# Kernel optimization log

Measured on AMD Instinct MI355X. Metric: run time of the kernel, lower is better.

The kernel has to match this reference:

```python
import jax, jax.numpy as jnp
import numpy as np
from jax import lax

NUM_HEADS = 4
ROPE_BASE = 10000.0


def _rope(x):
    # x: (b, h, w, c). Faithful to the torch RoPE: angles indexed by the h axis
    # with shape (h, c/2), which broadcasts against the w axis (requires h == w).
    b, h, w, c = x.shape
    k_max = c // 2
    theta = 1.0 / (ROPE_BASE ** (jnp.arange(k_max, dtype=x.dtype) / k_max))  # (c/2,)
    angles = jnp.arange(h, dtype=x.dtype)[:, None] * theta  # (h, c/2)
    cos, sin = jnp.cos(angles), jnp.sin(angles)
    xr = x.reshape(b, h, w, k_max, 2)
    re, im = xr[..., 0], xr[..., 1]
    # complex multiply (cos + i sin) * (re + i im); (h, c/2) broadcasts along w
    out_re = cos * re - sin * im
    out_im = sin * re + cos * im
    return jnp.stack([out_re, out_im], axis=-1).reshape(b, h, w, c)


def setup_inputs() -> dict:
    key = jax.random.key(0)
    k1, k2, k3, k4, k5 = jax.random.split(key, 5)
    b, c, h, w = 8, 512, 96, 96
    x = jax.random.normal(k1, (b, c, h, w), dtype=jnp.float32)
    W_qk = jax.random.normal(k2, (2 * c, c), dtype=jnp.float32) * (c ** -0.5)
    b_qk = jax.random.normal(k3, (2 * c,), dtype=jnp.float32) * 0.02
    lepe_w = jax.random.normal(k4, (c, 1, 3, 3), dtype=jnp.float32) * (1.0 / 3.0)
    lepe_b = jax.random.normal(k5, (c,), dtype=jnp.float32) * 0.02
    return {"x": x, "W_qk": W_qk, "b_qk": b_qk, "lepe_w": lepe_w, "lepe_b": lepe_b}


def reference(x, W_qk, b_qk, lepe_w, lepe_b):
    b, c, h, w = x.shape
    n = h * w
    heads = NUM_HEADS
    hd = c // heads

    xs = x.reshape(b, c, n).transpose(0, 2, 1)  # (b, n, c)
    qk = (xs @ W_qk.T + b_qk).reshape(b, n, 2, c)
    q = jax.nn.elu(qk[:, :, 0]) + 1.0  # (b, n, c)
    k = jax.nn.elu(qk[:, :, 1]) + 1.0
    v = xs

    q_rope = _rope(q.reshape(b, h, w, c)).reshape(b, n, heads, hd).transpose(0, 2, 1, 3)
    k_rope = _rope(k.reshape(b, h, w, c)).reshape(b, n, heads, hd).transpose(0, 2, 1, 3)

    # faithful flat reshape (b, n, c) -> (b, heads, n, hd) (splits the n axis)
    q2 = q.reshape(b, heads, n, hd)
    k2 = k.reshape(b, heads, n, hd)
    v2 = v.reshape(b, heads, n, hd)

    k_mean = k2.mean(axis=2, keepdims=True)  # (b, heads, 1, hd)
    z = 1.0 / (jnp.einsum('bhnd,bhmd->bhnm', q2, k_mean) + 1e-6)  # (b, heads, n, 1)

    scale = n ** -0.5
    kv = jnp.einsum('bhnd,bhne->bhde', k_rope * scale, v2 * scale)  # (b, heads, hd, hd)
    out = jnp.einsum('bhnd,bhde->bhne', q_rope, kv) * z  # (b, heads, n, hd)

    out = out.transpose(0, 2, 1, 3).reshape(b, n, c).transpose(0, 2, 1).reshape(b, c, h, w)

    # v2.reshape(b,h,w,c).permute(0,3,1,2) recovers the original (b, c, h, w) layout
    v_img = v2.reshape(b, h, w, c).transpose(0, 3, 1, 2)
    lepe = lax.conv_general_dilated(
        v_img, lepe_w, window_strides=(1, 1), padding='SAME',
        feature_group_count=c, dimension_numbers=('NCHW', 'OIHW', 'NCHW'))
    lepe = lepe + lepe_b[None, :, None, None]
    return out + lepe
```

## Files before the change

### kernel.cpp

```cpp
#include <hip/hip_runtime.h>
#include <hip/hip_bf16.h>
#include <cstdint>

#define BB 8
#define CC 512
#define HH 96
#define NN 9216
#define HEADS 4
#define HD 128
#define KMAX 256

typedef unsigned short ushort_t;
typedef __attribute__((ext_vector_type(8))) short bf16x8;
typedef __attribute__((ext_vector_type(4))) float f32x4;

__device__ __forceinline__ unsigned short f2bf(float f) {
  unsigned int u = __float_as_uint(f);
  u += 0x7fffu + ((u >> 16) & 1u);
  return (unsigned short)(u >> 16);
}
__device__ __forceinline__ float bf2f(unsigned short s) {
  return __uint_as_float(((unsigned int)s) << 16);
}
__device__ __forceinline__ unsigned int pk2(float lo, float hi) {
  return (unsigned int)f2bf(lo) | ((unsigned int)f2bf(hi) << 16);
}

__device__ __forceinline__ void gld16(const void* g, void* l) {
  __builtin_amdgcn_global_load_lds(
      (const __attribute__((address_space(1))) unsigned int*)(uintptr_t)g,
      (__attribute__((address_space(3))) unsigned int*)(unsigned int)(uintptr_t)l,
      16, 0, 0);
}

__global__ void rope_table_k(float* __restrict__ rope) {
  int t = blockIdx.x * 256 + threadIdx.x;
  if (t >= HH * KMAX) return;
  int col = t >> 8;
  int kk = t & (KMAX - 1);
  float theta = powf(10000.0f, -((float)kk) / (float)KMAX);
  float ang = (float)col * theta;
  float s, c;
  sincosf(ang, &s, &c);
  rope[2 * t] = c;
  rope[2 * t + 1] = s;
}

__global__ void conv_w_k(const float* __restrict__ W, unsigned short* __restrict__ Wbf) {
  int t = blockIdx.x * 256 + threadIdx.x;
  float4 v = *(const float4*)(W + (size_t)t * 4);
  unsigned int lo = (unsigned int)f2bf(v.x) | ((unsigned int)f2bf(v.y) << 16);
  unsigned int hi = (unsigned int)f2bf(v.z) | ((unsigned int)f2bf(v.w) << 16);
  *(uint2*)(Wbf + (size_t)t * 4) = make_uint2(lo, hi);
}

__global__ void transpose_all_k(const float* __restrict__ x, unsigned short* __restrict__ xt) {
  __shared__ unsigned short T[64 * 72];
  const int pos0 = blockIdx.x * 64;
  const int ch0 = blockIdx.y * 64;
  const int b = blockIdx.z;
  const int tid = threadIdx.x;
#pragma unroll
  for (int i = 0; i < 4; ++i) {
    int fi = i * 256 + tid;
    int ch = fi >> 4, p4 = fi & 15;
    float4 v = *(const float4*)(x + ((size_t)b * CC + ch0 + ch) * NN + pos0 + p4 * 4);
    T[(p4 * 4 + 0) * 72 + ch] = f2bf(v.x);
    T[(p4 * 4 + 1) * 72 + ch] = f2bf(v.y);
    T[(p4 * 4 + 2) * 72 + ch] = f2bf(v.z);
    T[(p4 * 4 + 3) * 72 + ch] = f2bf(v.w);
  }
  __syncthreads();
#pragma unroll
  for (int i = 0; i < 2; ++i) {
    int s = i * 256 + tid;
    int p = s >> 3, cc = s & 7;
    uint4 u = *(const uint4*)&T[p * 72 + cc * 8];
    *(uint4*)(xt + ((size_t)b * NN + pos0 + p) * CC + ch0 + cc * 8) = u;
  }
}

__launch_bounds__(256)
__global__ void gemm_qk_mfma(const unsigned short* __restrict__ xtall,
                             const unsigned short* __restrict__ Wbf,
                             const float* __restrict__ bqk,
                             unsigned short* __restrict__ qout,
                             unsigned short* __restrict__ kout) {
  __shared__ __align__(16) unsigned short sA[128 * 64];
  __shared__ __align__(16) unsigned short sB[128 * 64];
  const int flat = blockIdx.x;
  const int bn = (flat >> 3) & 7;
  const int g = ((flat >> 6) << 3) | (flat & 7);
  const int b = g / 72;
  const int m0 = (g - b * 72) * 128;
  const int tid = threadIdx.x;
  const int wv = tid >> 6, lane = tid & 63;
  const int j0 = bn * 128;
  const unsigned short* xt = xtall + (size_t)b * NN * CC;
  const int row = lane & 15, quad = lane >> 4;
  const int mt0 = (wv & 1) * 64, nt0 = (wv >> 1) * 64;
  f32x4 acc[4][4];
#pragma unroll
  for (int mi = 0; mi < 4; ++mi)
#pragma unroll
    for (int ni = 0; ni < 4; ++ni) acc[mi][ni] = (f32x4){0.f, 0.f, 0.f, 0.f};

  for (int kt = 0; kt < CC; kt += 64) {
#pragma unroll
    for (int it = 0; it < 4; ++it) {
      int s = it * 256 + tid;
      int srow = s >> 3;
      int sc = (s & 7) ^ (srow & 7);
      int ldsoff = (it * 256 + wv * 64) * 8;
      gld16(xt + (size_t)(m0 + srow) * CC + kt + sc * 8, &sA[ldsoff]);
      gld16(Wbf + (size_t)(j0 + srow) * CC + kt + sc * 8, &sB[ldsoff]);
    }
    __syncthreads();
#pragma unroll
    for (int ks = 0; ks < 2; ++ks) {
      bf16x8 af[4], bf[4];
      const int chunk = (ks * 4 + quad) ^ (row & 7);
#pragma unroll
      for (int mi = 0; mi < 4; ++mi)
        af[mi] = *(const bf16x8*)&sA[((mt0 + mi * 16 + row) * 8 + chunk) * 8];
#pragma unroll
      for (int ni = 0; ni < 4; ++ni)
        bf[ni] = *(const bf16x8*)&sB[((nt0 + ni * 16 + row) * 8 + chunk) * 8];
#pragma unroll
      for (int mi = 0; mi < 4; ++mi)
#pragma unroll
        for (int ni = 0; ni < 4; ++ni)
          acc[mi][ni] = __builtin_amdgcn_mfma_f32_16x16x32_bf16(af[mi], bf[ni], acc[mi][ni], 0, 0, 0);
    }
    __syncthreads();
  }
  unsigned short* dst = (j0 < CC) ? qout : kout;
  const int jl = (j0 & (CC - 1)) + nt0;
  float bj[4];
#pragma unroll
  for (int ni = 0; ni < 4; ++ni) bj[ni] = bqk[j0 + nt0 + ni * 16 + row];
#pragma unroll
  for (int mi = 0; mi < 4; ++mi) {
#pragma unroll
    for (int ni = 0; ni < 4; ++ni) {
#pragma unroll
      for (int r = 0; r < 4; ++r) {
        float v = acc[mi][ni][r] + bj[ni];
        v = v > 0.f ? v + 1.f : expm1f(v) + 1.f;
        int mrow = m0 + mt0 + mi * 16 + quad * 4 + r;
        dst[((size_t)b * NN + mrow) * CC + jl + ni * 16 + row] = f2bf(v);
      }
    }
  }
}

__global__ void kmean_p1_k(const unsigned short* __restrict__ kbf, float* __restrict__ part) {
  __shared__ float red[256];
  const int seg = blockIdx.x;
  const int bh = blockIdx.y;
  const int b = bh >> 2, head = bh & 3;
  const int tid = threadIdx.x;
  const int d = tid & 127, half = tid >> 7;
  const unsigned short* base =
      kbf + ((size_t)b * NN + head * 2304 + seg * 128 + half * 64) * CC + d;
  float sum = 0.f;
  for (int pp = 0; pp < 64; ++pp) {
    const unsigned short* rp = base + (size_t)pp * CC;
    sum += bf2f(rp[0]) + bf2f(rp[128]) + bf2f(rp[256]) + bf2f(rp[384]);
  }
  red[tid] = sum;
  __syncthreads();
  if (half == 0) part[((size_t)bh * 18 + seg) * 128 + d] = red[d] + red[d + 128];
}

__global__ void kmean_p2_k(const float* __restrict__ part, float* __restrict__ kmean) {
  int idx = blockIdx.x * 256 + threadIdx.x;
  int bh = idx >> 7, d = idx & 127;
  float s = 0.f;
#pragma unroll
  for (int i = 0; i < 18; ++i) s += part[((size_t)bh * 18 + i) * 128 + d];
  kmean[idx] = s * (1.0f / 9216.0f);
}

__global__ void z_k(const unsigned short* __restrict__ qbf, const float* __restrict__ kmean,
                    float* __restrict__ z) {
  const int wv = threadIdx.x >> 6, lane = threadIdx.x & 63;
  const int zbase = (blockIdx.x * 4 + wv) * 8;
  const int bh = zbase / NN;
  const int p0 = zbase % NN;
  const int b = bh >> 2, head = bh & 3;
  const float km0 = kmean[bh * 128 + lane * 2];
  const float km1 = kmean[bh * 128 + lane * 2 + 1];
#pragma unroll
  for (int it = 0; it < 8; ++it) {
    const int p = p0 + it;
    const int pos = head * 2304 + (p >> 2);
    const int chb = (p & 3) * 128;
    const unsigned short* qp = qbf + ((size_t)b * NN + pos) * CC + chb + lane * 2;
    float dot = bf2f(qp[0]) * km0 + bf2f(qp[1]) * km1;
#pragma unroll
    for (int off = 1; off < 64; off <<= 1) dot += __shfl_xor(dot, off, 64);
    if (lane == 0) z[zbase + it] = 1.0f / (dot + 1e-6f);
  }
}

__launch_bounds__(256, 2)
__global__ void kv_mfma_k(const unsigned short* __restrict__ kbf, const float* __restrict__ x,
                          const float* __restrict__ rope, float* __restrict__ kvp) {
  __shared__ __align__(16) unsigned short sK[128 * 64];
  const int s = blockIdx.x;
  const int bh = blockIdx.y;
  const int b = bh >> 2, head = bh & 3;
  const int tid = threadIdx.x;
  const int wv = tid >> 6, lane = tid & 63;
  const int row = lane & 15, quad = lane >> 4;
  const int e0 = (wv & 1) * 64, d0 = (wv >> 1) * 64;
  const int r = s >> 2;
  const int t0 = (s & 3) * 576;

  const int qg = tid & 7;
  const int dg = (tid >> 3) * 4;
  const unsigned short* kbase = kbf + (size_t)b * NN * CC + head * HD + dg;
  const int pairb = head * 64 + (dg >> 1);

  f32x4 acc[4][4];
#pragma unroll
  for (int mi = 0; mi < 4; ++mi)
#pragma unroll
    for (int ni = 0; ni < 4; ++ni) acc[mi][ni] = (f32x4){0.f, 0.f, 0.f, 0.f};

  for (int ck = 0; ck < 9; ++ck) {
    const int tc = t0 + ck * 64;
    float4 a0[8], a1[8];
#pragma unroll
    for (int mi = 0; mi < 4; ++mi)
#pragma unroll
      for (int ks = 0; ks < 2; ++ks) {
        const float* xp = x + (size_t)(b * CC + r * 128 + e0 + mi * 16 + row) * NN +
                          head * 2304 + tc + ks * 32 + quad * 8;
        a0[mi * 2 + ks] = *(const float4*)xp;
        a1[mi * 2 + ks] = *(const float4*)(xp + 4);
      }
    {
      int p = 4 * (tc + qg * 8) + r;
      int col = p % 96;
      float rw0[8], rw1[8], rw2[8], rw3[8];
#pragma unroll
      for (int j = 0; j < 8; ++j) {
        uint2 kv2 = *(const uint2*)(kbase + (size_t)p * CC);
        const float* rp = rope + ((size_t)col * KMAX + pairb) * 2;
        float4 cs = *(const float4*)rp;
        float re0 = bf2f((unsigned short)(kv2.x & 0xffffu));
        float im0 = bf2f((unsigned short)(kv2.x >> 16));
        float re1 = bf2f((unsigned short)(kv2.y & 0xffffu));
        float im1 = bf2f((unsigned short)(kv2.y >> 16));
        rw0[j] = cs.x * re0 - cs.y * im0;
        rw1[j] = cs.y * re0 + cs.x * im0;
        rw2[j] = cs.z * re1 - cs.w * im1;
        rw3[j] = cs.w * re1 + cs.z * im1;
        p += 4;
        col += 4;
        col = (col >= 96) ? col - 96 : col;
      }
#pragma unroll
      for (int rr = 0; rr < 4; ++rr) {
        const float* rw = (rr == 0) ? rw0 : (rr == 1) ? rw1 : (rr == 2) ? rw2 : rw3;
        const int d = dg + rr;
        uint4 pk;
        pk.x = pk2(rw[0], rw[1]);
        pk.y = pk2(rw[2], rw[3]);
        pk.z = pk2(rw[4], rw[5]);
        pk.w = pk2(rw[6], rw[7]);
        *(uint4*)&sK[(d * 8 + (qg ^ (d & 7))) * 8] = pk;
      }
    }
    __syncthreads();
#pragma unroll
    for (int ks = 0; ks < 2; ++ks) {
      bf16x8 bfr[4];
#pragma unroll
      for (int ni = 0; ni < 4; ++ni) {
        const int d = d0 + ni * 16 + row;
        const int o = (ks * 4 + quad) ^ (d & 7);
        bfr[ni] = *(const bf16x8*)&sK[(d * 8 + o) * 8];
      }
#pragma unroll
      for (int mi = 0; mi < 4; ++mi) {
        const int f = mi * 2 + ks;
        union { bf16x8 v; unsigned int u[4]; } af;
        af.u[0] = pk2(a0[f].x, a0[f].y);
        af.u[1] = pk2(a0[f].z, a0[f].w);
        af.u[2] = pk2(a1[f].x, a1[f].y);
        af.u[3] = pk2(a1[f].z, a1[f].w);
#pragma unroll
        for (int ni = 0; ni < 4; ++ni)
          acc[mi][ni] = __builtin_amdgcn_mfma_f32_16x16x32_bf16(af.v, bfr[ni], acc[mi][ni], 0, 0, 0);
      }
    }
    __syncthreads();
  }
  float* dst = kvp + (size_t)(s * 32 + bh) * (HD * HD);
#pragma unroll
  for (int mi = 0; mi < 4; ++mi) {
#pragma unroll
    for (int ni = 0; ni < 4; ++ni) {
#pragma unroll
      for (int rr = 0; rr < 4; ++rr) {
        const int e = e0 + mi * 16 + quad * 4 + rr;
        const int d = d0 + ni * 16 + row;
        dst[e * HD + d] = acc[mi][ni][rr];
      }
    }
  }
}

__global__ void kv_reduce_k(const float* __restrict__ kvp, unsigned short* __restrict__ kvtb) {
  int idx = blockIdx.x * 256 + threadIdx.x;
  float ssum = 0.f;
#pragma unroll
  for (int i = 0; i < 16; ++i) ssum += kvp[(size_t)i * (32 * HD * HD) + idx];
  kvtb[idx] = f2bf(ssum * (1.0f / 9216.0f));
}

__launch_bounds__(256)
__global__ void out_mfma_k(const unsigned short* __restrict__ qbf,
                           const unsigned short* __restrict__ kvtb,
                           const float* __restrict__ z, const float* __restrict__ rope,
                           float* __restrict__ out) {
  const int bh = blockIdx.y, b = bh >> 2, head = bh & 3;
  const int pos0 = blockIdx.x * 128;
  const int tid = threadIdx.x, wv = tid >> 6, lane = tid & 63;
  const int row = lane & 15, quad = lane >> 4;
  const int e0 = (wv & 1) * 64;
  const int p0 = (wv >> 1) * 64;
  f32x4 acc[4][4];
#pragma unroll
  for (int mi = 0; mi < 4; ++mi)
#pragma unroll
    for (int ni = 0; ni < 4; ++ni) acc[mi][ni] = (f32x4){0.f, 0.f, 0.f, 0.f};

  int posn[4], coln[4];
#pragma unroll
  for (int ni = 0; ni < 4; ++ni) {
    posn[ni] = pos0 + p0 + ni * 16 + row;
    coln[ni] = posn[ni] % 96;
  }

#pragma unroll
  for (int kt = 0; kt < HD; kt += 32) {
    bf16x8 af[4], bfr[4];
#pragma unroll
    for (int mi = 0; mi < 4; ++mi)
      af[mi] = *(const bf16x8*)&kvtb[((size_t)bh * HD + e0 + mi * 16 + row) * HD + kt + quad * 8];
#pragma unroll
    for (int ni = 0; ni < 4; ++ni) {
      const uint4 u = *(const uint4*)(qbf + ((size_t)b * NN + posn[ni]) * CC +
                                      head * HD + kt + quad * 8);
      const int pairb = head * 64 + (kt >> 1) + quad * 4;
      const float* rp = rope + ((size_t)coln[ni] * KMAX + pairb) * 2;
      float4 r0 = *(const float4*)rp;
      float4 r1 = *(const float4*)(rp + 4);
      unsigned int uu[4] = {u.x, u.y, u.z, u.w};
      float cs[8] = {r0.x, r0.y, r0.z, r0.w, r1.x, r1.y, r1.z, r1.w};
      bf16x8 bb;
#pragma unroll
      for (int pr = 0; pr < 4; ++pr) {
        float re = bf2f((unsigned short)(uu[pr] & 0xffffu));
        float im = bf2f((unsigned short)(uu[pr] >> 16));
        float c = cs[2 * pr], s = cs[2 * pr + 1];
        bb[2 * pr] = (short)f2bf(c * re - s * im);
        bb[2 * pr + 1] = (short)f2bf(s * re + c * im);
      }
      bfr[ni] = bb;
    }
#pragma unroll
    for (int mi = 0; mi < 4; ++mi)
#pragma unroll
      for (int ni = 0; ni < 4; ++ni)
        acc[mi][ni] = __builtin_amdgcn_mfma_f32_16x16x32_bf16(af[mi], bfr[ni], acc[mi][ni], 0, 0, 0);
  }
  float zv[4];
#pragma unroll
  for (int ni = 0; ni < 4; ++ni) zv[ni] = z[(size_t)bh * NN + posn[ni]];
#pragma unroll
  for (int mi = 0; mi < 4; ++mi) {
#pragma unroll
    for (int ni = 0; ni < 4; ++ni) {
#pragma unroll
      for (int r = 0; r < 4; ++r) {
        int e = e0 + mi * 16 + quad * 4 + r;
        out[((size_t)b * CC + head * HD + e) * NN + posn[ni]] = acc[mi][ni][r] * zv[ni];
      }
    }
  }
}

__global__ void lepe_k(const float* __restrict__ x, const float* __restrict__ lw,
                       const float* __restrict__ lb, float* __restrict__ out) {
  const int blk = blockIdx.x;
  const int bc = blk / 9;
  const int tile = blk - bc * 9;
  const int ch = bc & (CC - 1);
  const float* wp = lw + ch * 9;
  float w[9];
#pragma unroll
  for (int t = 0; t < 9; ++t) w[t] = wp[t];
  const float bias = lb[ch];
  const float* xp = x + (size_t)bc * NN;
  const int pos = tile * 1024 + threadIdx.x * 4;
  const int pi = pos / 96;
  const int pj = pos - pi * 96;

  float4 o = *(const float4*)(out + (size_t)bc * NN + pos);

  float a0 = bias, a1 = bias, a2 = bias, a3 = bias;
#pragma unroll
  for (int r = 0; r < 3; ++r) {
    const int y = pi + r - 1;
    if ((unsigned)y >= 96u) continue;
    const float* rowp = xp + y * 96 + pj;
    float4 M = *(const float4*)rowp;
    float Lv = (pj > 0) ? rowp[-1] : 0.f;
    float Rv = (pj < 92) ? rowp[4] : 0.f;
    const float w0 = w[r * 3 + 0], w1 = w[r * 3 + 1], w2 = w[r * 3 + 2];
    a0 += w0 * Lv + w1 * M.x + w2 * M.y;
    a1 += w0 * M.x + w1 * M.y + w2 * M.z;
    a2 += w0 * M.y + w1 * M.z + w2 * M.w;
    a3 += w0 * M.z + w1 * M.w + w2 * Rv;
  }
  o.x += a0; o.y += a1; o.z += a2; o.w += a3;
  *(float4*)(out + (size_t)bc * NN + pos) = o;
}

extern "C" void kernel_launch(void* const* d_in, const int* in_sizes, int n_in,
                              void* d_out, int out_size, void* d_ws, size_t ws_size,
                              hipStream_t stream) {
  const float* x = (const float*)d_in[0];
  const float* Wqk = (const float*)d_in[1];
  const float* bqk = (const float*)d_in[2];
  const float* lw = (const float*)d_in[3];
  const float* lb = (const float*)d_in[4];
  float* out = (float*)d_out;
  char* ws = (char*)d_ws;
  unsigned short* qbf = (unsigned short*)(ws);
  unsigned short* kbf = (unsigned short*)(ws + 75497472);
  float* rope = (float*)(ws + 150994944);
  float* kmean = (float*)(ws + 151191552);
  float* z = (float*)(ws + 151207936);
  float* kvp = (float*)(ws + 152387584);
  float* kmean_part = (float*)(ws + 152387584 + 16777216);
  unsigned short* kvtb = (unsigned short*)(ws + 185942016);
  unsigned short* Wbf = (unsigned short*)(ws + 188039168);
  unsigned short* xtb = (unsigned short*)d_out;

  conv_w_k<<<dim3(512), dim3(256), 0, stream>>>(Wqk, Wbf);
  rope_table_k<<<dim3(96), dim3(256), 0, stream>>>(rope);
  transpose_all_k<<<dim3(144, 8, 8), dim3(256), 0, stream>>>(x, xtb);
  gemm_qk_mfma<<<dim3(4608), dim3(256), 0, stream>>>(xtb, Wbf, bqk, qbf, kbf);
  kmean_p1_k<<<dim3(18, 32), dim3(256), 0, stream>>>(kbf, kmean_part);
  kmean_p2_k<<<dim3(16), dim3(256), 0, stream>>>(kmean_part, kmean);
  z_k<<<dim3(9216), dim3(256), 0, stream>>>(qbf, kmean, z);
  kv_mfma_k<<<dim3(16, 32), dim3(256), 0, stream>>>(kbf, x, rope, kvp);
  kv_reduce_k<<<dim3(2048), dim3(256), 0, stream>>>(kvp, kvtb);
  out_mfma_k<<<dim3(72, 32), dim3(256), 0, stream>>>(qbf, kvtb, z, rope, out);
  lepe_k<<<dim3(36864), dim3(256), 0, stream>>>(x, lw, lb, out);
}
```

Baseline: 723.2 us.

## Fuse k-mean reduction into QK GEMM epilogue and stage out_mfma through LDS

The QK GEMM swaps its operand roles so each lane holds four consecutive channels. That allows packed 8-byte bf16 stores and lets the kernel accumulate per-channel sums of k with shuffles and atomics, which replaces the two separate k-mean reduction kernels. The output kernel now loads its q tile into swizzled LDS once, and it transposes the result through LDS so the stores to the channel-major output are coalesced float4 writes instead of scattered scalar stores. This adds a memset, atomic contention, and extra barriers in the output kernel.

Result: no change. 713.2 us (-1.4%).

```diff
diff --git a/kernel.cpp b/kernel.cpp
--- a/kernel.cpp
+++ b/kernel.cpp
@@ -85,7 +85,8 @@
                              const unsigned short* __restrict__ Wbf,
                              const float* __restrict__ bqk,
                              unsigned short* __restrict__ qout,
-                             unsigned short* __restrict__ kout) {
+                             unsigned short* __restrict__ kout,
+                             float* __restrict__ ksum) {
   __shared__ __align__(16) unsigned short sA[128 * 64];
   __shared__ __align__(16) unsigned short sB[128 * 64];
   const int flat = blockIdx.x;
@@ -98,12 +99,12 @@
   const int j0 = bn * 128;
   const unsigned short* xt = xtall + (size_t)b * NN * CC;
   const int row = lane & 15, quad = lane >> 4;
-  const int mt0 = (wv & 1) * 64, nt0 = (wv >> 1) * 64;
+  const int jt0 = (wv & 1) * 64, pt0 = (wv >> 1) * 64;
   f32x4 acc[4][4];
 #pragma unroll
-  for (int mi = 0; mi < 4; ++mi)
-#pragma unroll
-    for (int ni = 0; ni < 4; ++ni) acc[mi][ni] = (f32x4){0.f, 0.f, 0.f, 0.f};
+  for (int ji = 0; ji < 4; ++ji)
+#pragma unroll
+    for (int pi = 0; pi < 4; ++pi) acc[ji][pi] = (f32x4){0.f, 0.f, 0.f, 0.f};
 
   for (int kt = 0; kt < CC; kt += 64) {
 #pragma unroll
@@ -118,79 +119,69 @@
     __syncthreads();
 #pragma unroll
     for (int ks = 0; ks < 2; ++ks) {
-      bf16x8 af[4], bf[4];
+      bf16x8 aw[4], ax[4];
       const int chunk = (ks * 4 + quad) ^ (row & 7);
 #pragma unroll
-      for (int mi = 0; mi < 4; ++mi)
-        af[mi] = *(const bf16x8*)&sA[((mt0 + mi * 16 + row) * 8 + chunk) * 8];
-#pragma unroll
-      for (int ni = 0; ni < 4; ++ni)
-        bf[ni] = *(const bf16x8*)&sB[((nt0 + ni * 16 + row) * 8 + chunk) * 8];
-#pragma unroll
-      for (int mi = 0; mi < 4; ++mi)
-#pragma unroll
-        for (int ni = 0; ni < 4; ++ni)
-          acc[mi][ni] = __builtin_amdgcn_mfma_f32_16x16x32_bf16(af[mi], bf[ni], acc[mi][ni], 0, 0, 0);
+      for (int ji = 0; ji < 4; ++ji)
+        aw[ji] = *(const bf16x8*)&sB[((jt0 + ji * 16 + row) * 8 + chunk) * 8];
+#pragma unroll
+      for (int pi = 0; pi < 4; ++pi)
+        ax[pi] = *(const bf16x8*)&sA[((pt0 + pi * 16 + row) * 8 + chunk) * 8];
+#pragma unroll
+      for (int ji = 0; ji < 4; ++ji)
+#pragma unroll
+        for (int pi = 0; pi < 4; ++pi)
+          acc[ji][pi] = __builtin_amdgcn_mfma_f32_16x16x32_bf16(aw[ji], ax[pi], acc[ji][pi], 0, 0, 0);
     }
     __syncthreads();
   }
   unsigned short* dst = (j0 < CC) ? qout : kout;
-  const int jl = (j0 & (CC - 1)) + nt0;
-  float bj[4];
-#pragma unroll
-  for (int ni = 0; ni < 4; ++ni) bj[ni] = bqk[j0 + nt0 + ni * 16 + row];
-#pragma unroll
-  for (int mi = 0; mi < 4; ++mi) {
-#pragma unroll
-    for (int ni = 0; ni < 4; ++ni) {
+  const int jl0 = j0 & (CC - 1);
+  const int pq = (m0 >> 7) / 18;
+#pragma unroll
+  for (int ji = 0; ji < 4; ++ji) {
+    const float4 bb = *(const float4*)&bqk[j0 + jt0 + ji * 16 + quad * 4];
+    const float bj[4] = {bb.x, bb.y, bb.z, bb.w};
+    float sacc[4] = {0.f, 0.f, 0.f, 0.f};
+#pragma unroll
+    for (int pi = 0; pi < 4; ++pi) {
+      float v[4];
 #pragma unroll
       for (int r = 0; r < 4; ++r) {
-        float v = acc[mi][ni][r] + bj[ni];
-        v = v > 0.f ? v + 1.f : expm1f(v) + 1.f;
-        int mrow = m0 + mt0 + mi * 16 + quad * 4 + r;
-        dst[((size_t)b * NN + mrow) * CC + jl + ni * 16 + row] = f2bf(v);
-      }
-    }
-  }
-}
-
-__global__ void kmean_p1_k(const unsigned short* __restrict__ kbf, float* __restrict__ part) {
-  __shared__ float red[256];
-  const int seg = blockIdx.x;
-  const int bh = blockIdx.y;
-  const int b = bh >> 2, head = bh & 3;
-  const int tid = threadIdx.x;
-  const int d = tid & 127, half = tid >> 7;
-  const unsigned short* base =
-      kbf + ((size_t)b * NN + head * 2304 + seg * 128 + half * 64) * CC + d;
-  float sum = 0.f;
-  for (int pp = 0; pp < 64; ++pp) {
-    const unsigned short* rp = base + (size_t)pp * CC;
-    sum += bf2f(rp[0]) + bf2f(rp[128]) + bf2f(rp[256]) + bf2f(rp[384]);
-  }
-  red[tid] = sum;
-  __syncthreads();
-  if (half == 0) part[((size_t)bh * 18 + seg) * 128 + d] = red[d] + red[d + 128];
-}
-
-__global__ void kmean_p2_k(const float* __restrict__ part, float* __restrict__ kmean) {
-  int idx = blockIdx.x * 256 + threadIdx.x;
-  int bh = idx >> 7, d = idx & 127;
-  float s = 0.f;
-#pragma unroll
-  for (int i = 0; i < 18; ++i) s += part[((size_t)bh * 18 + i) * 128 + d];
-  kmean[idx] = s * (1.0f / 9216.0f);
-}
-
-__global__ void z_k(const unsigned short* __restrict__ qbf, const float* __restrict__ kmean,
+        float t = acc[ji][pi][r] + bj[r];
+        v[r] = t > 0.f ? t + 1.f : __expf(t);
+        sacc[r] += v[r];
+      }
+      const int posm = m0 + pt0 + pi * 16 + row;
+      uint2 pkd = make_uint2(pk2(v[0], v[1]), pk2(v[2], v[3]));
+      *(uint2*)&dst[((size_t)b * NN + posm) * CC + jl0 + jt0 + ji * 16 + quad * 4] = pkd;
+    }
+    if (j0 >= CC) {
+#pragma unroll
+      for (int r = 0; r < 4; ++r) {
+        float s = sacc[r];
+        s += __shfl_xor(s, 1);
+        s += __shfl_xor(s, 2);
+        s += __shfl_xor(s, 4);
+        s += __shfl_xor(s, 8);
+        if (row == 0)
+          atomicAdd(&ksum[((size_t)b * 4 + pq) * 512 + jl0 + jt0 + ji * 16 + quad * 4 + r], s);
+      }
+    }
+  }
+}
+
+__global__ void z_k(const unsigned short* __restrict__ qbf, const float* __restrict__ ksum,
                     float* __restrict__ z) {
   const int wv = threadIdx.x >> 6, lane = threadIdx.x & 63;
   const int zbase = (blockIdx.x * 4 + wv) * 8;
   const int bh = zbase / NN;
   const int p0 = zbase % NN;
   const int b = bh >> 2, head = bh & 3;
-  const float km0 = kmean[bh * 128 + lane * 2];
-  const float km1 = kmean[bh * 128 + lane * 2 + 1];
+  const float* ks = ksum + (size_t)bh * 512;
+  const int d0 = lane * 2;
+  const float km0 = (ks[d0] + ks[d0 + 128] + ks[d0 + 256] + ks[d0 + 384]) * (1.0f / 9216.0f);
+  const float km1 = (ks[d0 + 1] + ks[d0 + 129] + ks[d0 + 257] + ks[d0 + 385]) * (1.0f / 9216.0f);
 #pragma unroll
   for (int it = 0; it < 8; ++it) {
     const int p = p0 + it;
@@ -327,12 +318,24 @@
                            const unsigned short* __restrict__ kvtb,
                            const float* __restrict__ z, const float* __restrict__ rope,
                            float* __restrict__ out) {
+  __shared__ __align__(16) float Ts[64 * 132];
+  unsigned short* sQ = (unsigned short*)Ts;
   const int bh = blockIdx.y, b = bh >> 2, head = bh & 3;
   const int pos0 = blockIdx.x * 128;
   const int tid = threadIdx.x, wv = tid >> 6, lane = tid & 63;
   const int row = lane & 15, quad = lane >> 4;
   const int e0 = (wv & 1) * 64;
   const int p0 = (wv >> 1) * 64;
+
+#pragma unroll
+  for (int it = 0; it < 8; ++it) {
+    const int s = it * 256 + tid;
+    const int srow = s >> 4, sc = s & 15;
+    const int scs = (sc & 8) | ((sc & 7) ^ (srow & 7));
+    gld16(qbf + ((size_t)b * NN + pos0 + srow) * CC + head * HD + scs * 8,
+          &sQ[(size_t)(it * 256 + wv * 64) * 8]);
+  }
+
   f32x4 acc[4][4];
 #pragma unroll
   for (int mi = 0; mi < 4; ++mi)
@@ -345,6 +348,7 @@
     posn[ni] = pos0 + p0 + ni * 16 + row;
     coln[ni] = posn[ni] % 96;
   }
+  __syncthreads();
 
 #pragma unroll
   for (int kt = 0; kt < HD; kt += 32) {
@@ -354,8 +358,10 @@
       af[mi] = *(const bf16x8*)&kvtb[((size_t)bh * HD + e0 + mi * 16 + row) * HD + kt + quad * 8];
 #pragma unroll
     for (int ni = 0; ni < 4; ++ni) {
-      const uint4 u = *(const uint4*)(qbf + ((size_t)b * NN + posn[ni]) * CC +
-                                      head * HD + kt + quad * 8);
+      const int posL = p0 + ni * 16 + row;
+      const int chb = (kt >> 3) + quad;
+      const int cl = (chb & 8) | ((chb & 7) ^ (posL & 7));
+      const uint4 u = *(const uint4*)&sQ[posL * 128 + cl * 8];
       const int pairb = head * 64 + (kt >> 1) + quad * 4;
       const float* rp = rope + ((size_t)coln[ni] * KMAX + pairb) * 2;
       float4 r0 = *(const float4*)rp;
@@ -379,19 +385,39 @@
       for (int ni = 0; ni < 4; ++ni)
         acc[mi][ni] = __builtin_amdgcn_mfma_f32_16x16x32_bf16(af[mi], bfr[ni], acc[mi][ni], 0, 0, 0);
   }
-  float zv[4];
-#pragma unroll
-  for (int ni = 0; ni < 4; ++ni) zv[ni] = z[(size_t)bh * NN + posn[ni]];
-#pragma unroll
-  for (int mi = 0; mi < 4; ++mi) {
-#pragma unroll
-    for (int ni = 0; ni < 4; ++ni) {
-#pragma unroll
-      for (int r = 0; r < 4; ++r) {
-        int e = e0 + mi * 16 + quad * 4 + r;
-        out[((size_t)b * CC + head * HD + e) * NN + posn[ni]] = acc[mi][ni][r] * zv[ni];
-      }
-    }
+#pragma unroll
+  for (int ni = 0; ni < 4; ++ni) {
+    const float zn = z[(size_t)bh * NN + posn[ni]];
+#pragma unroll
+    for (int mi = 0; mi < 4; ++mi)
+#pragma unroll
+      for (int r = 0; r < 4; ++r) acc[mi][ni][r] *= zn;
+  }
+  __syncthreads();
+
+#pragma unroll
+  for (int h = 0; h < 2; ++h) {
+    if ((wv & 1) == h) {
+#pragma unroll
+      for (int mi = 0; mi < 4; ++mi)
+#pragma unroll
+        for (int ni = 0; ni < 4; ++ni)
+#pragma unroll
+          for (int r = 0; r < 4; ++r) {
+            const int eL = mi * 16 + quad * 4 + r;
+            const int p = p0 + ni * 16 + row;
+            Ts[eL * 132 + p] = acc[mi][ni][r];
+          }
+    }
+    __syncthreads();
+#pragma unroll
+    for (int i = 0; i < 8; ++i) {
+      const int eL = i * 8 + (tid >> 5);
+      const int c = tid & 31;
+      const float4 vv = *(const float4*)&Ts[eL * 132 + c * 4];
+      *(float4*)&out[((size_t)b * CC + head * HD + h * 64 + eL) * NN + pos0 + c * 4] = vv;
+    }
+    __syncthreads();
   }
 }
 
@@ -445,21 +471,19 @@
   unsigned short* qbf = (unsigned short*)(ws);
   unsigned short* kbf = (unsigned short*)(ws + 75497472);
   float* rope = (float*)(ws + 150994944);
-  float* kmean = (float*)(ws + 151191552);
   float* z = (float*)(ws + 151207936);
   float* kvp = (float*)(ws + 152387584);
-  float* kmean_part = (float*)(ws + 152387584 + 16777216);
+  float* ksum = (float*)(ws + 152387584);
   unsigned short* kvtb = (unsigned short*)(ws + 185942016);
   unsigned short* Wbf = (unsigned short*)(ws + 188039168);
   unsigned short* xtb = (unsigned short*)d_out;
 
+  hipMemsetAsync(ksum, 0, (size_t)BB * 4 * 512 * sizeof(float), stream);
   conv_w_k<<<dim3(512), dim3(256), 0, stream>>>(Wqk, Wbf);
   rope_table_k<<<dim3(96), dim3(256), 0, stream>>>(rope);
   transpose_all_k<<<dim3(144, 8, 8), dim3(256), 0, stream>>>(x, xtb);
-  gemm_qk_mfma<<<dim3(4608), dim3(256), 0, stream>>>(xtb, Wbf, bqk, qbf, kbf);
-  kmean_p1_k<<<dim3(18, 32), dim3(256), 0, stream>>>(kbf, kmean_part);
-  kmean_p2_k<<<dim3(16), dim3(256), 0, stream>>>(kmean_part, kmean);
-  z_k<<<dim3(9216), dim3(256), 0, stream>>>(qbf, kmean, z);
+  gemm_qk_mfma<<<dim3(4608), dim3(256), 0, stream>>>(xtb, Wbf, bqk, qbf, kbf, ksum);
+  z_k<<<dim3(9216), dim3(256), 0, stream>>>(qbf, ksum, z);
   kv_mfma_k<<<dim3(16, 32), dim3(256), 0, stream>>>(kbf, x, rope, kvp);
   kv_reduce_k<<<dim3(2048), dim3(256), 0, stream>>>(kvp, kvtb);
   out_mfma_k<<<dim3(72, 32), dim3(256), 0, stream>>>(qbf, kvtb, z, rope, out);
```
